# Kernel optimization log

Hardware: AMD Instinct MI355X
Metric: run time of the kernel (lower is better)

The kernel has to match this reference:

```python
import jax, jax.numpy as jnp
import numpy as np

B, S, D = 2, 2048, 1024
H, DH = 16, 64  # n_heads, d_head = d_model // n_heads


def setup_inputs() -> dict:
    key = jax.random.key(0)
    ks = jax.random.split(key, 12)
    scale = 1.0 / np.sqrt(D)
    return {
        "queries": jax.random.normal(ks[0], (B, S, D), jnp.float32),
        "keys": jax.random.normal(ks[1], (B, S, D), jnp.float32),
        "values": jax.random.normal(ks[2], (B, S, D), jnp.float32),
        "mask": jax.random.randint(ks[3], (1, 1, S, S), 0, 2, jnp.int32),
        "Wq": jax.random.normal(ks[4], (D, D), jnp.float32) * scale,
        "bq": jnp.zeros((D,), jnp.float32),
        "Wk": jax.random.normal(ks[5], (D, D), jnp.float32) * scale,
        "bk": jnp.zeros((D,), jnp.float32),
        "Wv": jax.random.normal(ks[6], (D, D), jnp.float32) * scale,
        "bv": jnp.zeros((D,), jnp.float32),
        "Wo": jax.random.normal(ks[7], (D, D), jnp.float32) * scale,
        "bo": jnp.zeros((D,), jnp.float32),
    }


def _split_proj(x):
    # (B, ?, H, DH) reshape then permute -> (B, H, ?, DH)
    b = x.shape[0]
    return x.reshape(b, -1, H, DH).transpose(0, 2, 1, 3)


def reference(queries, keys, values, mask, Wq, bq, Wk, bk, Wv, bv, Wo, bo):
    q = queries @ Wq.T + bq
    k = keys @ Wk.T + bk
    v = values @ Wv.T + bv
    # NOTE: original source applies split_proj to queries twice (faithful repro)
    q = _split_proj(_split_proj(q))
    k = _split_proj(k)
    v = _split_proj(v)
    scores = jnp.einsum('bhqd,bhkd->bhqk', q, k) / jnp.sqrt(jnp.float32(DH))
    scores = scores + mask.astype(scores.dtype) * (-1e9)
    attn = jax.nn.softmax(scores, axis=-1)
    out = jnp.einsum('bhqk,bhkd->bhqd', attn, v)  # (B,H,S,DH)
    out = out.transpose(0, 2, 1, 3).reshape(out.shape[0], -1, D)
    return out @ Wo.T + bo
```

## Files before the change

### kernel.cpp

```cpp
#include <hip/hip_runtime.h>
#include <hip/hip_bf16.h>
#include <cstddef>
#include <cstdint>


typedef __attribute__((ext_vector_type(8))) short bf16x8;
typedef __attribute__((ext_vector_type(4))) float f32x4;

__device__ __forceinline__ void gl_lds16(const void* g, void* l) {
    __builtin_amdgcn_global_load_lds(
        (const __attribute__((address_space(1))) void*)g,
        (__attribute__((address_space(3))) void*)l, 16, 0, 0);
}

__global__ __launch_bounds__(256) void convert_all(
    const float* __restrict__ q, const float* __restrict__ k, const float* __restrict__ v,
    const float* __restrict__ wq, const float* __restrict__ wk,
    const float* __restrict__ wv, const float* __restrict__ wo,
    __hip_bfloat16* __restrict__ dq, __hip_bfloat16* __restrict__ dk,
    __hip_bfloat16* __restrict__ dv, __hip_bfloat16* __restrict__ dwq,
    __hip_bfloat16* __restrict__ dwk, __hip_bfloat16* __restrict__ dwv,
    __hip_bfloat16* __restrict__ dwo)
{
    const int bid = blockIdx.x;
    const float* s; __hip_bfloat16* d; int base;
    if      (bid < 2048) { s = q;  d = dq;  base = bid; }
    else if (bid < 4096) { s = k;  d = dk;  base = bid - 2048; }
    else if (bid < 6144) { s = v;  d = dv;  base = bid - 4096; }
    else if (bid < 6656) { s = wq; d = dwq; base = bid - 6144; }
    else if (bid < 7168) { s = wk; d = dwk; base = bid - 6656; }
    else if (bid < 7680) { s = wv; d = dwv; base = bid - 7168; }
    else                 { s = wo; d = dwo; base = bid - 7680; }
    const size_t i = (size_t)base * 256 + threadIdx.x;
    const float4* sp = (const float4*)s + i * 2;
    float4 v0 = sp[0], v1 = sp[1];
    union { __hip_bfloat16 h[8]; int4 qd; } u;
    u.h[0] = __float2bfloat16(v0.x); u.h[1] = __float2bfloat16(v0.y);
    u.h[2] = __float2bfloat16(v0.z); u.h[3] = __float2bfloat16(v0.w);
    u.h[4] = __float2bfloat16(v1.x); u.h[5] = __float2bfloat16(v1.y);
    u.h[6] = __float2bfloat16(v1.z); u.h[7] = __float2bfloat16(v1.w);
    *((int4*)d + i) = u.qd;
}

__global__ __launch_bounds__(256) void packmask(const int* __restrict__ mask,
                                                unsigned long long* __restrict__ mbits)
{
    const int wid  = (blockIdx.x * 256 + threadIdx.x) >> 6;
    const int lane = threadIdx.x & 63;
    const int qr = wid >> 5, w64 = wid & 31;
    const int m = mask[(size_t)qr * 2048 + w64 * 64 + lane];
    const unsigned long long bal = __ballot(m != 0);
    if (lane == 0) mbits[(size_t)qr * 32 + w64] = bal;
}

template <typename OutT>
__device__ __forceinline__ void gemm_body(
    const __hip_bfloat16* __restrict__ A, const __hip_bfloat16* __restrict__ Bm,
    const float* __restrict__ bias, OutT* __restrict__ C,
    int N, int m0, int n0, int brow,
    __hip_bfloat16* As, __hip_bfloat16* Bs)
{
    const int t = threadIdx.x, lane = t & 63, w = t >> 6;
    const int l15 = lane & 15, g = lane >> 4;
    const int wr = w >> 1, wc = w & 1;

    f32x4 acc[4][4] = {};

    for (int k0 = 0; k0 < 1024; k0 += 64) {
        __syncthreads();
        #pragma unroll
        for (int it = 0; it < 4; ++it) {
            const int chunk = it * 256 + w * 64 + lane;
            const int row = chunk >> 3, c = chunk & 7;
            gl_lds16(A  + (size_t)(m0 + row) * 1024 + k0 + c * 8, (char*)As + chunk * 16);
            gl_lds16(Bm + (size_t)(n0 + row) * 1024 + k0 + c * 8, (char*)Bs + chunk * 16);
        }
        __syncthreads();
        #pragma unroll
        for (int kk = 0; kk < 64; kk += 32) {
            bf16x8 af[4], bfr[4];
            #pragma unroll
            for (int i = 0; i < 4; ++i)
                af[i] = *(const bf16x8*)((const char*)As + (wr * 64 + i * 16 + l15) * 128 + kk * 2 + g * 16);
            #pragma unroll
            for (int j = 0; j < 4; ++j)
                bfr[j] = *(const bf16x8*)((const char*)Bs + (wc * 64 + j * 16 + l15) * 128 + kk * 2 + g * 16);
            #pragma unroll
            for (int i = 0; i < 4; ++i)
                #pragma unroll
                for (int j = 0; j < 4; ++j)
                    acc[i][j] = __builtin_amdgcn_mfma_f32_16x16x32_bf16(af[i], bfr[j], acc[i][j], 0, 0, 0);
        }
    }

    #pragma unroll
    for (int i = 0; i < 4; ++i) {
        const int m = m0 + wr * 64 + i * 16 + g * 4;
        #pragma unroll
        for (int j = 0; j < 4; ++j) {
            const int n = n0 + wc * 64 + j * 16 + l15;
            const float bc = brow ? 0.f : bias[n];
            #pragma unroll
            for (int r = 0; r < 4; ++r) {
                const float v = acc[i][j][r] + (brow ? bias[m + r] : bc);
                C[(size_t)(m + r) * N + n] = (OutT)v;
            }
        }
    }
}

__global__ __launch_bounds__(256) void qkv_gemm(
    const __hip_bfloat16* __restrict__ qin, const __hip_bfloat16* __restrict__ kin,
    const __hip_bfloat16* __restrict__ vin,
    const __hip_bfloat16* __restrict__ Wqb, const __hip_bfloat16* __restrict__ Wkb,
    const __hip_bfloat16* __restrict__ Wvb,
    const float* __restrict__ bq, const float* __restrict__ bk, const float* __restrict__ bv,
    __hip_bfloat16* __restrict__ qbuf, __hip_bfloat16* __restrict__ kbuf,
    __hip_bfloat16* __restrict__ vtb)
{
    __shared__ __align__(16) __hip_bfloat16 As[128 * 64];
    __shared__ __align__(16) __hip_bfloat16 Bs[128 * 64];
    const int z = blockIdx.z;
    if (z == 0)
        gemm_body(qin, Wqb, bq, qbuf, 1024, blockIdx.y * 128, blockIdx.x * 128, 0, As, Bs);
    else if (z == 1)
        gemm_body(kin, Wkb, bk, kbuf, 1024, blockIdx.y * 128, blockIdx.x * 128, 0, As, Bs);
    else
        gemm_body(Wvb, vin, bv, vtb, 4096, blockIdx.x * 128, blockIdx.y * 128, 1, As, Bs);
}

__global__ __launch_bounds__(256) void out_gemm(
    const __hip_bfloat16* __restrict__ A, const __hip_bfloat16* __restrict__ Bm,
    const float* __restrict__ bias, float* __restrict__ C)
{
    __shared__ __align__(16) __hip_bfloat16 As[128 * 64];
    __shared__ __align__(16) __hip_bfloat16 Bs[128 * 64];
    gemm_body(A, Bm, bias, C, 1024, blockIdx.y * 128, blockIdx.x * 128, 0, As, Bs);
}

__global__ __launch_bounds__(256, 6) void attn_mfma(
    const __hip_bfloat16* __restrict__ qb,
    const __hip_bfloat16* __restrict__ kb,
    const __hip_bfloat16* __restrict__ vt,
    const unsigned long long* __restrict__ mbits,
    __hip_bfloat16* __restrict__ ctx)
{
    __shared__ __align__(16) __hip_bfloat16 Ks[64 * 64];
    __shared__ __align__(16) __hip_bfloat16 Vs[64 * 64];
    __shared__ __align__(16) __hip_bfloat16 Pb[4][16 * 64];

    const int t = threadIdx.x, lane = t & 63, w = t >> 6;
    const int l15 = lane & 15, g = lane >> 4;

    const int bid = blockIdx.x;
    const int xcd = bid & 7, i = bid >> 3;
    const int bh = xcd * 4 + (i >> 5), qt = i & 31;
    const int b = bh >> 4, a = bh & 15;
    const int q0 = qt * 64;
    const int hq = q0 >> 7;

    constexpr float SC_LOG2E = 0.18033688011112042f;
    constexpr float OFFC     = -17.312340490667561f;
    constexpr float MASKB    = -1.0e9f;

    const int qrow = w * 16 + l15;
    const int s = ((q0 & 64) + qrow) * 16 + a;
    bf16x8 qreg[2];
    #pragma unroll
    for (int half = 0; half < 2; ++half)
        qreg[half] = *(const bf16x8*)&qb[(size_t)(b * 2048 + s) * 1024 + hq * 64 + (half * 4 + g) * 8];

    f32x4 accd[4] = {};
    float l_r = 0.f;
    const int qg = q0 + qrow;

    for (int kt = 0; kt < 32; ++kt) {
        __syncthreads();
        #pragma unroll
        for (int it = 0; it < 2; ++it) {
            const int c = it * 256 + t;
            const int row = c >> 3, cc = c & 7;
            const int cs = cc ^ (row & 7);
            gl_lds16(kb + (size_t)(b * 2048 + kt * 64 + row) * 1024 + a * 64 + cs * 8,
                     (char*)Ks + c * 16);
            gl_lds16(vt + (size_t)(a * 64 + row) * 4096 + b * 2048 + kt * 64 + cs * 8,
                     (char*)Vs + c * 16);
        }
        const uint2 mw = *(const uint2*)&mbits[(size_t)qg * 32 + kt];
        __syncthreads();

        f32x4 sf[4] = {};
        #pragma unroll
        for (int half = 0; half < 2; ++half) {
            const int kc = half * 4 + g;
            #pragma unroll
            for (int nf = 0; nf < 4; ++nf) {
                const int krow = nf * 16 + l15;
                const bf16x8 kf = *(const bf16x8*)((const char*)Ks + krow * 128 + ((kc ^ (krow & 7)) << 4));
                sf[nf] = __builtin_amdgcn_mfma_f32_16x16x32_bf16(kf, qreg[half], sf[nf], 0, 0, 0);
            }
        }

        float psum = 0.f;
        #pragma unroll
        for (int nf = 0; nf < 4; ++nf) {
            const unsigned word = (nf & 2) ? mw.y : mw.x;
            const int bsh = ((nf & 1) << 4) + (g << 2);
            float pr[4];
            #pragma unroll
            for (int r = 0; r < 4; ++r) {
                const bool msk = (word >> (bsh + r)) & 1u;
                pr[r] = exp2f(fmaf(sf[nf][r], SC_LOG2E, msk ? MASKB : OFFC));
            }
            psum += (pr[0] + pr[1]) + (pr[2] + pr[3]);
            __hip_bfloat16 h0 = __float2bfloat16(pr[0]), h1 = __float2bfloat16(pr[1]);
            __hip_bfloat16 h2 = __float2bfloat16(pr[2]), h3 = __float2bfloat16(pr[3]);
            const unsigned w0 = (unsigned)*(unsigned short*)&h0 | ((unsigned)*(unsigned short*)&h1 << 16);
            const unsigned w1 = (unsigned)*(unsigned short*)&h2 | ((unsigned)*(unsigned short*)&h3 << 16);
            char* pb = (char*)Pb + w * 2048 + l15 * 128 +
                       (((2 * nf + (g >> 1)) ^ (l15 & 7)) << 4) + ((g & 1) << 3);
            *(uint2*)pb = make_uint2(w0, w1);
        }
        psum += __shfl_xor(psum, 16);
        psum += __shfl_xor(psum, 32);
        l_r += psum;

        #pragma unroll
        for (int jj = 0; jj < 2; ++jj) {
            const bf16x8 pa = *(const bf16x8*)((const char*)Pb + w * 2048 + l15 * 128 +
                                               (((4 * jj + g) ^ (l15 & 7)) << 4));
            #pragma unroll
            for (int df = 0; df < 4; ++df) {
                const int vrow = df * 16 + l15;
                const bf16x8 vf = *(const bf16x8*)((const char*)Vs + vrow * 128 +
                                                   (((4 * jj + g) ^ (vrow & 7)) << 4));
                accd[df] = __builtin_amdgcn_mfma_f32_16x16x32_bf16(pa, vf, accd[df], 0, 0, 0);
            }
        }
    }

    #pragma unroll
    for (int r = 0; r < 4; ++r) {
        const float lq = __shfl(l_r, (g << 2) + r);
        const float inv = 1.0f / lq;
        const int q = q0 + w * 16 + (g << 2) + r;
        #pragma unroll
        for (int df = 0; df < 4; ++df)
            ctx[(size_t)(b * 2048 + q) * 1024 + (a << 6) + df * 16 + l15] =
                __float2bfloat16(accd[df][r] * inv);
    }
}

extern "C" void kernel_launch(void* const* d_in, const int* in_sizes, int n_in,
                              void* d_out, int out_size, void* d_ws, size_t ws_size,
                              hipStream_t stream)
{
    const float* queries = (const float*)d_in[0];
    const float* keys    = (const float*)d_in[1];
    const float* values  = (const float*)d_in[2];
    const int*   mask    = (const int*)  d_in[3];
    const float* Wq = (const float*)d_in[4];
    const float* bq = (const float*)d_in[5];
    const float* Wk = (const float*)d_in[6];
    const float* bk = (const float*)d_in[7];
    const float* Wv = (const float*)d_in[8];
    const float* bv = (const float*)d_in[9];
    const float* Wo = (const float*)d_in[10];
    const float* bo = (const float*)d_in[11];

    const size_t NM = (size_t)4096 * 1024;
    const size_t NW = (size_t)1024 * 1024;
    __hip_bfloat16* p = (__hip_bfloat16*)d_ws;
    __hip_bfloat16* qin = p;  p += NM;
    __hip_bfloat16* kin = p;  p += NM;
    __hip_bfloat16* vin = p;  p += NM;
    __hip_bfloat16* Wqb = p;  p += NW;
    __hip_bfloat16* Wkb = p;  p += NW;
    __hip_bfloat16* Wvb = p;  p += NW;
    __hip_bfloat16* Wob = p;  p += NW;
    __hip_bfloat16* qbuf = p; p += NM;
    __hip_bfloat16* kbuf = p; p += NM;
    __hip_bfloat16* vtb  = p; p += NM;
    unsigned long long* mbits = (unsigned long long*)p;
    __hip_bfloat16* ctxb = qin;

    convert_all<<<dim3(8192), dim3(256), 0, stream>>>(
        queries, keys, values, Wq, Wk, Wv, Wo,
        qin, kin, vin, Wqb, Wkb, Wvb, Wob);
    packmask<<<dim3(16384), dim3(256), 0, stream>>>(mask, mbits);

    qkv_gemm<<<dim3(8, 32, 3), dim3(256), 0, stream>>>(
        qin, kin, vin, Wqb, Wkb, Wvb, bq, bk, bv, qbuf, kbuf, vtb);

    attn_mfma<<<dim3(1024), dim3(256), 0, stream>>>(qbuf, kbuf, vtb, mbits, ctxb);

    out_gemm<<<dim3(8, 32), dim3(256), 0, stream>>>(ctxb, Wob, bo, (float*)d_out);
}
```

Baseline: 190.5 us.

## Split attention keys across two wave groups with double-buffered LDS and register P

The attention kernel now uses 512-thread blocks that each handle 128 queries. Two groups of four waves each process half of the key tiles, and their partial outputs and row sums are merged through shared memory at the end. K/V tiles are double-buffered with async global-to-LDS loads to overlap loading with compute. P is kept in registers using permlane swaps instead of an LDS round trip, and the row sums come from an MFMA against a ones vector. Separately, the output GEMM is templated to use 64-row tiles so it launches twice as many blocks, and the fp32-to-bf16 conversion is factored into a helper. The larger blocks and the 64 KB of shared memory may reduce occupancy.

```diff
diff --git a/kernel.cpp b/kernel.cpp
--- a/kernel.cpp
+++ b/kernel.cpp
@@ -11,6 +11,16 @@
     __builtin_amdgcn_global_load_lds(
         (const __attribute__((address_space(1))) void*)g,
         (__attribute__((address_space(3))) void*)l, 16, 0, 0);
+}
+
+__device__ __forceinline__ int4 cvt8(const float* __restrict__ src) {
+    const float4 v0 = *(const float4*)src, v1 = *(const float4*)(src + 4);
+    union { __hip_bfloat16 h[8]; int4 q; } u;
+    u.h[0] = __float2bfloat16(v0.x); u.h[1] = __float2bfloat16(v0.y);
+    u.h[2] = __float2bfloat16(v0.z); u.h[3] = __float2bfloat16(v0.w);
+    u.h[4] = __float2bfloat16(v1.x); u.h[5] = __float2bfloat16(v1.y);
+    u.h[6] = __float2bfloat16(v1.z); u.h[7] = __float2bfloat16(v1.w);
+    return u.q;
 }
 
 __global__ __launch_bounds__(256) void convert_all(
@@ -32,14 +42,7 @@
     else if (bid < 7680) { s = wv; d = dwv; base = bid - 7168; }
     else                 { s = wo; d = dwo; base = bid - 7680; }
     const size_t i = (size_t)base * 256 + threadIdx.x;
-    const float4* sp = (const float4*)s + i * 2;
-    float4 v0 = sp[0], v1 = sp[1];
-    union { __hip_bfloat16 h[8]; int4 qd; } u;
-    u.h[0] = __float2bfloat16(v0.x); u.h[1] = __float2bfloat16(v0.y);
-    u.h[2] = __float2bfloat16(v0.z); u.h[3] = __float2bfloat16(v0.w);
-    u.h[4] = __float2bfloat16(v1.x); u.h[5] = __float2bfloat16(v1.y);
-    u.h[6] = __float2bfloat16(v1.z); u.h[7] = __float2bfloat16(v1.w);
-    *((int4*)d + i) = u.qd;
+    *((int4*)d + i) = cvt8(s + i * 8);
 }
 
 __global__ __launch_bounds__(256) void packmask(const int* __restrict__ mask,
@@ -53,7 +56,7 @@
     if (lane == 0) mbits[(size_t)qr * 32 + w64] = bal;
 }
 
-template <typename OutT>
+template <int MR, typename OutT>
 __device__ __forceinline__ void gemm_body(
     const __hip_bfloat16* __restrict__ A, const __hip_bfloat16* __restrict__ Bm,
     const float* __restrict__ bias, OutT* __restrict__ C,
@@ -63,30 +66,34 @@
     const int t = threadIdx.x, lane = t & 63, w = t >> 6;
     const int l15 = lane & 15, g = lane >> 4;
     const int wr = w >> 1, wc = w & 1;
-
-    f32x4 acc[4][4] = {};
+    constexpr int NI = MR / 32;
+
+    f32x4 acc[NI][4] = {};
 
     for (int k0 = 0; k0 < 1024; k0 += 64) {
         __syncthreads();
         #pragma unroll
+        for (int it = 0; it < NI; ++it) {
+            const int c = it * 256 + t, row = c >> 3, c8 = c & 7;
+            gl_lds16(A + (size_t)(m0 + row) * 1024 + k0 + c8 * 8, (char*)As + c * 16);
+        }
+        #pragma unroll
         for (int it = 0; it < 4; ++it) {
-            const int chunk = it * 256 + w * 64 + lane;
-            const int row = chunk >> 3, c = chunk & 7;
-            gl_lds16(A  + (size_t)(m0 + row) * 1024 + k0 + c * 8, (char*)As + chunk * 16);
-            gl_lds16(Bm + (size_t)(n0 + row) * 1024 + k0 + c * 8, (char*)Bs + chunk * 16);
+            const int c = it * 256 + t, row = c >> 3, c8 = c & 7;
+            gl_lds16(Bm + (size_t)(n0 + row) * 1024 + k0 + c8 * 8, (char*)Bs + c * 16);
         }
         __syncthreads();
         #pragma unroll
         for (int kk = 0; kk < 64; kk += 32) {
-            bf16x8 af[4], bfr[4];
-            #pragma unroll
-            for (int i = 0; i < 4; ++i)
-                af[i] = *(const bf16x8*)((const char*)As + (wr * 64 + i * 16 + l15) * 128 + kk * 2 + g * 16);
+            bf16x8 af[NI], bfr[4];
+            #pragma unroll
+            for (int i = 0; i < NI; ++i)
+                af[i] = *(const bf16x8*)((const char*)As + (wr * (MR / 2) + i * 16 + l15) * 128 + kk * 2 + g * 16);
             #pragma unroll
             for (int j = 0; j < 4; ++j)
                 bfr[j] = *(const bf16x8*)((const char*)Bs + (wc * 64 + j * 16 + l15) * 128 + kk * 2 + g * 16);
             #pragma unroll
-            for (int i = 0; i < 4; ++i)
+            for (int i = 0; i < NI; ++i)
                 #pragma unroll
                 for (int j = 0; j < 4; ++j)
                     acc[i][j] = __builtin_amdgcn_mfma_f32_16x16x32_bf16(af[i], bfr[j], acc[i][j], 0, 0, 0);
@@ -94,8 +101,8 @@
     }
 
     #pragma unroll
-    for (int i = 0; i < 4; ++i) {
-        const int m = m0 + wr * 64 + i * 16 + g * 4;
+    for (int i = 0; i < NI; ++i) {
+        const int m = m0 + wr * (MR / 2) + i * 16 + g * 4;
         #pragma unroll
         for (int j = 0; j < 4; ++j) {
             const int n = n0 + wc * 64 + j * 16 + l15;
@@ -122,132 +129,199 @@
     __shared__ __align__(16) __hip_bfloat16 Bs[128 * 64];
     const int z = blockIdx.z;
     if (z == 0)
-        gemm_body(qin, Wqb, bq, qbuf, 1024, blockIdx.y * 128, blockIdx.x * 128, 0, As, Bs);
+        gemm_body<128>(qin, Wqb, bq, qbuf, 1024, blockIdx.y * 128, blockIdx.x * 128, 0, As, Bs);
     else if (z == 1)
-        gemm_body(kin, Wkb, bk, kbuf, 1024, blockIdx.y * 128, blockIdx.x * 128, 0, As, Bs);
+        gemm_body<128>(kin, Wkb, bk, kbuf, 1024, blockIdx.y * 128, blockIdx.x * 128, 0, As, Bs);
     else
-        gemm_body(Wvb, vin, bv, vtb, 4096, blockIdx.x * 128, blockIdx.y * 128, 1, As, Bs);
+        gemm_body<128>(Wvb, vin, bv, vtb, 4096, blockIdx.x * 128, blockIdx.y * 128, 1, As, Bs);
 }
 
 __global__ __launch_bounds__(256) void out_gemm(
     const __hip_bfloat16* __restrict__ A, const __hip_bfloat16* __restrict__ Bm,
     const float* __restrict__ bias, float* __restrict__ C)
 {
-    __shared__ __align__(16) __hip_bfloat16 As[128 * 64];
+    __shared__ __align__(16) __hip_bfloat16 As[64 * 64];
     __shared__ __align__(16) __hip_bfloat16 Bs[128 * 64];
-    gemm_body(A, Bm, bias, C, 1024, blockIdx.y * 128, blockIdx.x * 128, 0, As, Bs);
-}
-
-__global__ __launch_bounds__(256, 6) void attn_mfma(
+    gemm_body<64>(A, Bm, bias, C, 1024, blockIdx.y * 64, blockIdx.x * 128, 0, As, Bs);
+}
+
+__global__ __launch_bounds__(512, 4) void attn_mfma(
     const __hip_bfloat16* __restrict__ qb,
     const __hip_bfloat16* __restrict__ kb,
     const __hip_bfloat16* __restrict__ vt,
     const unsigned long long* __restrict__ mbits,
     __hip_bfloat16* __restrict__ ctx)
 {
-    __shared__ __align__(16) __hip_bfloat16 Ks[64 * 64];
-    __shared__ __align__(16) __hip_bfloat16 Vs[64 * 64];
-    __shared__ __align__(16) __hip_bfloat16 Pb[4][16 * 64];
+    __shared__ __align__(16) char smem[65536];
 
     const int t = threadIdx.x, lane = t & 63, w = t >> 6;
+    const int grp = w >> 2, wl = w & 3;
     const int l15 = lane & 15, g = lane >> 4;
+    const int tloc = t & 255;
 
     const int bid = blockIdx.x;
-    const int xcd = bid & 7, i = bid >> 3;
-    const int bh = xcd * 4 + (i >> 5), qt = i & 31;
+    const int xcd = bid & 7, ii = bid >> 3;
+    const int bh = (xcd << 2) + (ii >> 4), qt = ii & 15;
     const int b = bh >> 4, a = bh & 15;
-    const int q0 = qt * 64;
-    const int hq = q0 >> 7;
+    const int q0 = qt * 128;
+    const int kt0 = grp * 16;
 
     constexpr float SC_LOG2E = 0.18033688011112042f;
     constexpr float OFFC     = -17.312340490667561f;
     constexpr float MASKB    = -1.0e9f;
 
-    const int qrow = w * 16 + l15;
-    const int s = ((q0 & 64) + qrow) * 16 + a;
-    bf16x8 qreg[2];
+    bf16x8 qreg[2][2];
+    int qgl[2];
     #pragma unroll
-    for (int half = 0; half < 2; ++half)
-        qreg[half] = *(const bf16x8*)&qb[(size_t)(b * 2048 + s) * 1024 + hq * 64 + (half * 4 + g) * 8];
-
-    f32x4 accd[4] = {};
-    float l_r = 0.f;
-    const int qg = q0 + qrow;
-
-    for (int kt = 0; kt < 32; ++kt) {
+    for (int u = 0; u < 2; ++u) {
+        const int qg = q0 + wl * 32 + u * 16 + l15;
+        qgl[u] = qg;
+        const int srow = (qg & 127) * 16 + a;
+        #pragma unroll
+        for (int half = 0; half < 2; ++half)
+            qreg[u][half] = *(const bf16x8*)&qb[(size_t)(b * 2048 + srow) * 1024 + qt * 64 + (half * 4 + g) * 8];
+    }
+
+    const int srow0 = tloc >> 3, scc = tloc & 7;
+    const int scs = scc ^ (srow0 & 7);
+    const char* kSrc = (const char*)(kb + (size_t)(b * 2048 + kt0 * 64 + srow0) * 1024 + a * 64 + scs * 8);
+    const char* vSrc = (const char*)(vt + (size_t)(a * 64 + srow0) * 4096 + b * 2048 + kt0 * 64 + scs * 8);
+    char* kDst = smem + grp * 16384 + tloc * 16;
+    char* vDst = smem + 32768 + grp * 16384 + tloc * 16;
+
+    auto stage = [&](int bufn) {
+        gl_lds16(kSrc,          kDst + bufn * 8192);
+        gl_lds16(kSrc + 65536,  kDst + bufn * 8192 + 4096);
+        gl_lds16(vSrc,          vDst + bufn * 8192);
+        gl_lds16(vSrc + 262144, vDst + bufn * 8192 + 4096);
+        kSrc += 131072;
+        vSrc += 128;
+    };
+
+    int kofs[2][4], vofs[2][4];
+    #pragma unroll
+    for (int x = 0; x < 2; ++x)
+        #pragma unroll
+        for (int nf = 0; nf < 4; ++nf) {
+            const int rr = nf * 16 + l15;
+            const int sw = ((x * 4 + g) ^ (rr & 7)) << 4;
+            kofs[x][nf] = grp * 16384 + rr * 128 + sw;
+            vofs[x][nf] = 32768 + grp * 16384 + rr * 128 + sw;
+        }
+
+    const unsigned long long* mbP0 = mbits + (size_t)qgl[0] * 32 + kt0;
+    const unsigned long long* mbP1 = mbits + (size_t)qgl[1] * 32 + kt0;
+
+    bf16x8 ones;
+    #pragma unroll
+    for (int e = 0; e < 8; ++e) ones[e] = (short)0x3F80;
+
+    f32x4 accd[2][4] = {};
+    f32x4 accl[2] = {};
+
+    stage(0);
+    __syncthreads();
+
+    auto do_tile = [&](int buf, bool doStage) {
+        if (doStage) stage(buf ^ 1);
+        const uint2 mw0 = *(const uint2*)mbP0; ++mbP0;
+        const uint2 mw1 = *(const uint2*)mbP1; ++mbP1;
+
+        f32x4 sf[2][4] = {};
+        #pragma unroll
+        for (int half = 0; half < 2; ++half)
+            #pragma unroll
+            for (int nf = 0; nf < 4; ++nf) {
+                const bf16x8 kf = *(const bf16x8*)(smem + kofs[half][nf] + buf * 8192);
+                sf[0][nf] = __builtin_amdgcn_mfma_f32_16x16x32_bf16(kf, qreg[0][half], sf[0][nf], 0, 0, 0);
+                sf[1][nf] = __builtin_amdgcn_mfma_f32_16x16x32_bf16(kf, qreg[1][half], sf[1][nf], 0, 0, 0);
+            }
+
+        unsigned Wrd[2][4][2];
+        #pragma unroll
+        for (int u = 0; u < 2; ++u) {
+            const uint2 mwv = u ? mw1 : mw0;
+            #pragma unroll
+            for (int nf = 0; nf < 4; ++nf) {
+                const unsigned word = (nf & 2) ? mwv.y : mwv.x;
+                const int bsh = ((nf & 1) << 4) + (g << 2);
+                float pr[4];
+                #pragma unroll
+                for (int r = 0; r < 4; ++r) {
+                    const bool msk = (word >> (bsh + r)) & 1u;
+                    pr[r] = exp2f(fmaf(sf[u][nf][r], SC_LOG2E, msk ? MASKB : OFFC));
+                }
+                unsigned w0, w1;
+                asm("v_cvt_pk_bf16_f32 %0, %1, %2" : "=v"(w0) : "v"(pr[0]), "v"(pr[1]));
+                asm("v_cvt_pk_bf16_f32 %0, %1, %2" : "=v"(w1) : "v"(pr[2]), "v"(pr[3]));
+                Wrd[u][nf][0] = w0;
+                Wrd[u][nf][1] = w1;
+            }
+        }
+
+        #pragma unroll
+        for (int jj = 0; jj < 2; ++jj) {
+            bf16x8 paf[2];
+            #pragma unroll
+            for (int u = 0; u < 2; ++u) {
+                unsigned f0 = Wrd[u][2 * jj][0], f2 = Wrd[u][2 * jj + 1][0];
+                unsigned f1 = Wrd[u][2 * jj][1], f3 = Wrd[u][2 * jj + 1][1];
+                asm volatile("v_permlane32_swap_b32 %0, %1" : "+v"(f0), "+v"(f2));
+                asm volatile("v_permlane16_swap_b32 %0, %1" : "+v"(f0), "+v"(f2));
+                asm volatile("v_permlane32_swap_b32 %0, %1" : "+v"(f1), "+v"(f3));
+                asm volatile("v_permlane16_swap_b32 %0, %1" : "+v"(f1), "+v"(f3));
+                union { unsigned uw[4]; bf16x8 v; } uu;
+                uu.uw[0] = f0; uu.uw[1] = f1; uu.uw[2] = f2; uu.uw[3] = f3;
+                paf[u] = uu.v;
+                accl[u] = __builtin_amdgcn_mfma_f32_16x16x32_bf16(paf[u], ones, accl[u], 0, 0, 0);
+            }
+            #pragma unroll
+            for (int df = 0; df < 4; ++df) {
+                const bf16x8 vf = *(const bf16x8*)(smem + vofs[jj][df] + buf * 8192);
+                accd[0][df] = __builtin_amdgcn_mfma_f32_16x16x32_bf16(paf[0], vf, accd[0][df], 0, 0, 0);
+                accd[1][df] = __builtin_amdgcn_mfma_f32_16x16x32_bf16(paf[1], vf, accd[1][df], 0, 0, 0);
+            }
+        }
         __syncthreads();
-        #pragma unroll
-        for (int it = 0; it < 2; ++it) {
-            const int c = it * 256 + t;
-            const int row = c >> 3, cc = c & 7;
-            const int cs = cc ^ (row & 7);
-            gl_lds16(kb + (size_t)(b * 2048 + kt * 64 + row) * 1024 + a * 64 + cs * 8,
-                     (char*)Ks + c * 16);
-            gl_lds16(vt + (size_t)(a * 64 + row) * 4096 + b * 2048 + kt * 64 + cs * 8,
-                     (char*)Vs + c * 16);
-        }
-        const uint2 mw = *(const uint2*)&mbits[(size_t)qg * 32 + kt];
-        __syncthreads();
-
-        f32x4 sf[4] = {};
-        #pragma unroll
-        for (int half = 0; half < 2; ++half) {
-            const int kc = half * 4 + g;
-            #pragma unroll
-            for (int nf = 0; nf < 4; ++nf) {
-                const int krow = nf * 16 + l15;
-                const bf16x8 kf = *(const bf16x8*)((const char*)Ks + krow * 128 + ((kc ^ (krow & 7)) << 4));
-                sf[nf] = __builtin_amdgcn_mfma_f32_16x16x32_bf16(kf, qreg[half], sf[nf], 0, 0, 0);
-            }
-        }
-
-        float psum = 0.f;
-        #pragma unroll
-        for (int nf = 0; nf < 4; ++nf) {
-            const unsigned word = (nf & 2) ? mw.y : mw.x;
-            const int bsh = ((nf & 1) << 4) + (g << 2);
-            float pr[4];
+    };
+
+    #pragma unroll 1
+    for (int it2 = 0; it2 < 8; ++it2) {
+        do_tile(0, true);
+        do_tile(1, it2 != 7);
+    }
+
+    float* cmbO = (float*)smem;
+    float* cmbL = (float*)(smem + 32768);
+    if (grp == 0) {
+        #pragma unroll
+        for (int u = 0; u < 2; ++u)
             #pragma unroll
             for (int r = 0; r < 4; ++r) {
-                const bool msk = (word >> (bsh + r)) & 1u;
-                pr[r] = exp2f(fmaf(sf[nf][r], SC_LOG2E, msk ? MASKB : OFFC));
-            }
-            psum += (pr[0] + pr[1]) + (pr[2] + pr[3]);
-            __hip_bfloat16 h0 = __float2bfloat16(pr[0]), h1 = __float2bfloat16(pr[1]);
-            __hip_bfloat16 h2 = __float2bfloat16(pr[2]), h3 = __float2bfloat16(pr[3]);
-            const unsigned w0 = (unsigned)*(unsigned short*)&h0 | ((unsigned)*(unsigned short*)&h1 << 16);
-            const unsigned w1 = (unsigned)*(unsigned short*)&h2 | ((unsigned)*(unsigned short*)&h3 << 16);
-            char* pb = (char*)Pb + w * 2048 + l15 * 128 +
-                       (((2 * nf + (g >> 1)) ^ (l15 & 7)) << 4) + ((g & 1) << 3);
-            *(uint2*)pb = make_uint2(w0, w1);
-        }
-        psum += __shfl_xor(psum, 16);
-        psum += __shfl_xor(psum, 32);
-        l_r += psum;
-
-        #pragma unroll
-        for (int jj = 0; jj < 2; ++jj) {
-            const bf16x8 pa = *(const bf16x8*)((const char*)Pb + w * 2048 + l15 * 128 +
-                                               (((4 * jj + g) ^ (l15 & 7)) << 4));
-            #pragma unroll
-            for (int df = 0; df < 4; ++df) {
-                const int vrow = df * 16 + l15;
-                const bf16x8 vf = *(const bf16x8*)((const char*)Vs + vrow * 128 +
-                                                   (((4 * jj + g) ^ (vrow & 7)) << 4));
-                accd[df] = __builtin_amdgcn_mfma_f32_16x16x32_bf16(pa, vf, accd[df], 0, 0, 0);
-            }
-        }
-    }
-
-    #pragma unroll
-    for (int r = 0; r < 4; ++r) {
-        const float lq = __shfl(l_r, (g << 2) + r);
-        const float inv = 1.0f / lq;
-        const int q = q0 + w * 16 + (g << 2) + r;
-        #pragma unroll
-        for (int df = 0; df < 4; ++df)
-            ctx[(size_t)(b * 2048 + q) * 1024 + (a << 6) + df * 16 + l15] =
-                __float2bfloat16(accd[df][r] * inv);
+                const int row = wl * 32 + u * 16 + (g << 2) + r;
+                #pragma unroll
+                for (int df = 0; df < 4; ++df)
+                    cmbO[row * 64 + df * 16 + l15] = accd[u][df][r];
+                if (l15 == 0) cmbL[row] = accl[u][r];
+            }
+    }
+    __syncthreads();
+    if (grp == 1) {
+        #pragma unroll
+        for (int u = 0; u < 2; ++u)
+            #pragma unroll
+            for (int r = 0; r < 4; ++r) {
+                const int row = wl * 32 + u * 16 + (g << 2) + r;
+                const float lsum = accl[u][r] + cmbL[row];
+                const float inv = 1.0f / lsum;
+                const int qglob = q0 + row;
+                #pragma unroll
+                for (int df = 0; df < 4; ++df) {
+                    const float o = accd[u][df][r] + cmbO[row * 64 + df * 16 + l15];
+                    ctx[(size_t)(b * 2048 + qglob) * 1024 + (a << 6) + df * 16 + l15] =
+                        __float2bfloat16(o * inv);
+                }
+            }
     }
 }
 
@@ -292,7 +366,7 @@
     qkv_gemm<<<dim3(8, 32, 3), dim3(256), 0, stream>>>(
         qin, kin, vin, Wqb, Wkb, Wvb, bq, bk, bv, qbuf, kbuf, vtb);
 
-    attn_mfma<<<dim3(1024), dim3(256), 0, stream>>>(qbuf, kbuf, vtb, mbits, ctxb);
-
-    out_gemm<<<dim3(8, 32), dim3(256), 0, stream>>>(ctxb, Wob, bo, (float*)d_out);
-}
+    attn_mfma<<<dim3(512), dim3(512), 0, stream>>>(qbuf, kbuf, vtb, mbits, ctxb);
+
+    out_gemm<<<dim3(8, 64), dim3(256), 0, stream>>>(ctxb, Wob, bo, (float*)d_out);
+}
```

After: 171.3 us. 1.11x faster.
